# Kernel tuning notes

Hardware: AMD Instinct MI355X
Metric: run time of the kernel (lower is better)

## Reference

```python
import jax, jax.numpy as jnp
import numpy as np
import math

B = 50        # graphs per batch
NPG = 2000    # nodes per graph
EPG = 12000   # edges per graph
F_IN = 256
NHID = 128
RATIO = 0.8


def setup_inputs() -> dict:
    key = jax.random.key(0)
    ks = jax.random.split(key, 12)
    N = B * NPG
    src_loc = jax.random.randint(ks[0], (B, EPG), 0, NPG)
    dst_loc = jax.random.randint(ks[1], (B, EPG), 0, NPG)
    off = (jnp.arange(B) * NPG)[:, None]
    edge_index = jnp.stack([(src_loc + off).reshape(-1), (dst_loc + off).reshape(-1)]).astype(jnp.int32)

    def lin(k, fi, fo):
        return (jax.random.normal(k, (fi, fo), jnp.float32) / np.sqrt(fi).astype(np.float32))

    return {
        "x": jax.random.normal(ks[2], (N, F_IN), jnp.float32),
        "W1": lin(ks[3], F_IN, NHID), "b1": jnp.zeros(NHID, jnp.float32),
        "Ws1": lin(ks[4], NHID, 1), "bs1": jnp.zeros(1, jnp.float32),
        "W2": lin(ks[5], NHID, NHID), "b2": jnp.zeros(NHID, jnp.float32),
        "Ws2": lin(ks[6], NHID, 1), "bs2": jnp.zeros(1, jnp.float32),
        "W3": lin(ks[7], NHID, NHID), "b3": jnp.zeros(NHID, jnp.float32),
        "Ws3": lin(ks[8], NHID, 1), "bs3": jnp.zeros(1, jnp.float32),
        "Wl": lin(ks[9], 2 * NHID, NHID), "bl": jnp.zeros(NHID, jnp.float32),
        "edge_index": edge_index,
    }


def gcn_conv(x, W, b, src, dst, w, N):
    # PyG GCNConv: D^{-1/2} (A + I) D^{-1/2} X W + b, deg from edge weights + self loop
    h = x @ W
    deg = jax.ops.segment_sum(w, dst, num_segments=N) + 1.0
    dis = jax.lax.rsqrt(deg)
    norm = w * dis[src] * dis[dst]                       # [E]
    agg = jax.ops.segment_sum(h[src] * norm[:, None], dst, num_segments=N)
    return agg + h / deg[:, None] + b                    # self-loop norm = 1/deg


def sag_pool(x, src, dst, w, Ws, bs, n_per_graph):
    N = x.shape[0]
    k = math.ceil(RATIO * n_per_graph)
    score = gcn_conv(x, Ws, bs, src, dst, w, N)[:, 0]    # [N]
    _, topi = jax.lax.top_k(score.reshape(B, n_per_graph), k)
    perm = (topi + (jnp.arange(B) * n_per_graph)[:, None]).reshape(-1)
    x_new = x[perm] * jnp.tanh(score[perm])[:, None]
    # filter_adj: keep edges whose endpoints survive, reindex; dropped edges -> weight 0
    mapping = jnp.full((N,), -1, jnp.int32).at[perm].set(jnp.arange(B * k, dtype=jnp.int32))
    ns, nd = mapping[src], mapping[dst]
    valid = (ns >= 0) & (nd >= 0) & (w > 0)
    return (x_new, jnp.where(valid, ns, 0), jnp.where(valid, nd, 0),
            jnp.where(valid, w, jnp.zeros((), x.dtype)), k)


def readout(x, n):
    # global max pool || global mean pool (equal-size graphs, nodes grouped per graph)
    xr = x.reshape(B, n, -1)
    return jnp.concatenate([xr.max(axis=1), xr.mean(axis=1)], axis=-1)


def reference(x, W1, b1, Ws1, bs1, W2, b2, Ws2, bs2, W3, b3, Ws3, bs3, Wl, bl, edge_index):
    src, dst = edge_index[0], edge_index[1]
    w = jnp.ones(src.shape[0], x.dtype)
    n = NPG
    x = jax.nn.relu(gcn_conv(x, W1, b1, src, dst, w, B * n))
    x, src, dst, w, n = sag_pool(x, src, dst, w, Ws1, bs1, n)
    x1 = readout(x, n)
    x = jax.nn.relu(gcn_conv(x, W2, b2, src, dst, w, B * n))
    x, src, dst, w, n = sag_pool(x, src, dst, w, Ws2, bs2, n)
    x2 = readout(x, n)
    x = jax.nn.relu(gcn_conv(x, W3, b3, src, dst, w, B * n))
    x, src, dst, w, n = sag_pool(x, src, dst, w, Ws3, bs3, n)
    x3 = readout(x, n)
    return jax.nn.relu((x1 + x2 + x3) @ Wl + bl)
```

## Files before the change

### kernel.cpp

```cpp
#include <hip/hip_runtime.h>
#include <math.h>

#define B_GRAPHS 50
#define NPG0     2000
#define EPG      12000
#define F_IN_C   256
#define NHID     128
#define N0       (B_GRAPHS * NPG0)
#define NE       (B_GRAPHS * EPG)
#define RSEG     16
#define GSLOTS   7
#define CPAD     136

typedef _Float16 f16x8 __attribute__((ext_vector_type(8)));
typedef float    f32x4 __attribute__((ext_vector_type(4)));

static inline int cdiv(int a, int b) { return (a + b - 1) / b; }

__global__ void k_fill_start(int* __restrict__ cnt, float* __restrict__ accum) {
    int i = blockIdx.x * 256 + threadIdx.x;
    if (i < N0) cnt[i] = 0;
    if (i < B_GRAPHS * 256) accum[i] = 0.f;
}

__global__ void k_init_edges(const int* __restrict__ ei, int* __restrict__ esrc,
                             int* __restrict__ edst, float* __restrict__ ew,
                             int* __restrict__ cnt) {
    int e = blockIdx.x * 256 + threadIdx.x;
    if (e < NE) {
        int d = ei[NE + e];
        esrc[e] = ei[e]; edst[e] = d; ew[e] = 1.0f;
        atomicAdd(&cnt[d], 1);
    }
}

__global__ void k_cvt_all(const float* __restrict__ W1, const float* __restrict__ W2,
                          const float* __restrict__ W3, _Float16* __restrict__ WT1,
                          _Float16* __restrict__ WT2, _Float16* __restrict__ WT3) {
    int t = blockIdx.x * 256 + threadIdx.x;
    if (t < 128 * 256) {
        int n = t >> 8, kk = t & 255;
        WT1[t] = (_Float16)W1[kk * 128 + n];
    } else if (t < 128 * 256 + 128 * 128) {
        int u = t - 32768; int n = u >> 7, kk = u & 127;
        WT2[u] = (_Float16)W2[kk * 128 + n];
    } else {
        int u = t - 49152; int n = u >> 7, kk = u & 127;
        WT3[u] = (_Float16)W3[kk * 128 + n];
    }
}

template<int FP32IN, int F, int GATHER>
__global__ __launch_bounds__(256) void k_gemm_ws(const void* __restrict__ Xin,
                                                 const _Float16* __restrict__ WT,
                                                 const int* __restrict__ perm,
                                                 const float* __restrict__ gate,
                                                 _Float16* __restrict__ H, int N) {
    constexpr int SMEMSZ = (F * 128 > 128 * CPAD) ? F * 128 : 128 * CPAD;
    __shared__ _Float16 smem[SMEMSZ];
    const int tid  = threadIdx.x;
    const int wave = tid >> 6, lane = tid & 63;
    const int quad = lane >> 4, l16 = lane & 15;
    const int m_blk = blockIdx.x * 128;

    constexpr int K8 = F / 8;
#pragma unroll
    for (int c = tid; c < 128 * K8; c += 256) {
        int n = c / K8, k8 = c - n * K8;
        f16x8 v = *(const f16x8*)&WT[(size_t)c * 8];
        *(f16x8*)&smem[n * F + ((k8 ^ (n & 7)) << 3)] = v;
    }
    __syncthreads();

    f32x4 acc[2][8];
#pragma unroll
    for (int i = 0; i < 2; ++i)
#pragma unroll
        for (int j = 0; j < 8; ++j) acc[i][j] = {0.f, 0.f, 0.f, 0.f};

    int row0 = m_blk + wave * 32 + l16;
    int row1 = row0 + 16;
    if (row0 > N - 1) row0 = N - 1;
    if (row1 > N - 1) row1 = N - 1;
    _Float16 g0 = (_Float16)1.0f, g1 = (_Float16)1.0f;
    if (GATHER) {
        g0 = (_Float16)gate[row0]; g1 = (_Float16)gate[row1];
        row0 = perm[row0]; row1 = perm[row1];
    }
    const int sx = l16 & 7;
    constexpr int NKQ = F / 32;

    if (FP32IN) {
        constexpr int PD = (NKQ < 4) ? NKQ : 4;
        const float* base0 = (const float*)Xin + (size_t)row0 * F + quad * 8;
        const float* base1 = (const float*)Xin + (size_t)row1 * F + quad * 8;
        float4 p0[PD][2], p1[PD][2];
#pragma unroll
        for (int i = 0; i < PD; ++i) {
            p0[i][0] = ((const float4*)(base0 + i * 32))[0];
            p0[i][1] = ((const float4*)(base0 + i * 32))[1];
            p1[i][0] = ((const float4*)(base1 + i * 32))[0];
            p1[i][1] = ((const float4*)(base1 + i * 32))[1];
        }
#pragma unroll
        for (int kq = 0; kq < NKQ; ++kq) {
            const int b = kq % PD;
            float4 f0 = p0[b][0], f1 = p0[b][1], h0 = p1[b][0], h1 = p1[b][1];
            if (kq + PD < NKQ) {
                p0[b][0] = ((const float4*)(base0 + (kq + PD) * 32))[0];
                p0[b][1] = ((const float4*)(base0 + (kq + PD) * 32))[1];
                p1[b][0] = ((const float4*)(base1 + (kq + PD) * 32))[0];
                p1[b][1] = ((const float4*)(base1 + (kq + PD) * 32))[1];
            }
            f16x8 af0 = (f16x8){(_Float16)f0.x,(_Float16)f0.y,(_Float16)f0.z,(_Float16)f0.w,
                                (_Float16)f1.x,(_Float16)f1.y,(_Float16)f1.z,(_Float16)f1.w};
            f16x8 af1 = (f16x8){(_Float16)h0.x,(_Float16)h0.y,(_Float16)h0.z,(_Float16)h0.w,
                                (_Float16)h1.x,(_Float16)h1.y,(_Float16)h1.z,(_Float16)h1.w};
            f16x8 bf[8];
#pragma unroll
            for (int j = 0; j < 8; ++j)
                bf[j] = *(const f16x8*)&smem[(j * 16 + l16) * F + ((((kq << 2) + quad) ^ sx) << 3)];
#pragma unroll
            for (int j = 0; j < 8; ++j) {
                acc[0][j] = __builtin_amdgcn_mfma_f32_16x16x32_f16(af0, bf[j], acc[0][j], 0, 0, 0);
                acc[1][j] = __builtin_amdgcn_mfma_f32_16x16x32_f16(af1, bf[j], acc[1][j], 0, 0, 0);
            }
        }
    } else {
        const _Float16* base0 = (const _Float16*)Xin + (size_t)row0 * F + quad * 8;
        const _Float16* base1 = (const _Float16*)Xin + (size_t)row1 * F + quad * 8;
        f16x8 q0[NKQ], q1[NKQ];
#pragma unroll
        for (int i = 0; i < NKQ; ++i) {
            q0[i] = *(const f16x8*)(base0 + i * 32);
            q1[i] = *(const f16x8*)(base1 + i * 32);
        }
#pragma unroll
        for (int kq = 0; kq < NKQ; ++kq) {
            f16x8 af0 = q0[kq], af1 = q1[kq];
            if (GATHER) { af0 = af0 * g0; af1 = af1 * g1; }
            f16x8 bf[8];
#pragma unroll
            for (int j = 0; j < 8; ++j)
                bf[j] = *(const f16x8*)&smem[(j * 16 + l16) * F + ((((kq << 2) + quad) ^ sx) << 3)];
#pragma unroll
            for (int j = 0; j < 8; ++j) {
                acc[0][j] = __builtin_amdgcn_mfma_f32_16x16x32_f16(af0, bf[j], acc[0][j], 0, 0, 0);
                acc[1][j] = __builtin_amdgcn_mfma_f32_16x16x32_f16(af1, bf[j], acc[1][j], 0, 0, 0);
            }
        }
    }
    __syncthreads();

    _Float16* sC = smem;
    const int rw = wave * 32;
#pragma unroll
    for (int i = 0; i < 2; ++i)
#pragma unroll
        for (int j = 0; j < 8; ++j)
#pragma unroll
            for (int g = 0; g < 4; ++g)
                sC[(rw + i * 16 + quad * 4 + g) * CPAD + j * 16 + l16] = (_Float16)acc[i][j][g];
    __syncthreads();
    {
        int rr = tid >> 1;
        int gr = m_blk + rr;
        if (gr < N) {
            _Float16* Hr = H + (size_t)gr * 128 + (tid & 1) * 64;
            const _Float16* Sr = sC + rr * CPAD + (tid & 1) * 64;
#pragma unroll
            for (int c = 0; c < 8; ++c)
                *(f16x8*)&Hr[c * 8] = *(const f16x8*)&Sr[c * 8];
        }
    }
}

__global__ __launch_bounds__(256) void k_scan(const int* __restrict__ cnt,
                                              int* __restrict__ offs,
                                              int* __restrict__ cursor, int npg) {
    __shared__ int ch[256];
    int b = blockIdx.x, tid = threadIdx.x;
    int per = (npg + 255) >> 8;
    int base = b * npg;
    int s0 = tid * per;
    int s1 = s0 + per; if (s1 > npg) s1 = npg; if (s0 > npg) s0 = npg;
    int s = 0;
    for (int i = s0; i < s1; ++i) s += cnt[base + i];
    ch[tid] = s;
    __syncthreads();
    for (int d = 1; d < 256; d <<= 1) {
        int t = ch[tid] + ((tid >= d) ? ch[tid - d] : 0);
        __syncthreads();
        ch[tid] = t;
        __syncthreads();
    }
    int run = b * EPG + ch[tid] - s;
    for (int i = s0; i < s1; ++i) {
        offs[base + i] = run; cursor[base + i] = run;
        run += cnt[base + i];
    }
}

__global__ void k_fill_csr(const int* __restrict__ esrc, const int* __restrict__ edst,
                           const float* __restrict__ ew, const int* __restrict__ cnt,
                           int* __restrict__ cursor, int* __restrict__ csr_src,
                           float* __restrict__ csr_norm) {
    int e = blockIdx.x * 256 + threadIdx.x;
    if (e < NE) {
        if (ew[e] > 0.f) {
            int sN = esrc[e], d = edst[e];
            int pos = atomicAdd(&cursor[d], 1);
            csr_src[pos] = sN;
            csr_norm[pos] = rsqrtf((float)(cnt[sN] + 1)) * rsqrtf((float)(cnt[d] + 1));
        }
    }
}

__global__ __launch_bounds__(256) void k_agg(const _Float16* __restrict__ H,
                                             const int* __restrict__ csr_src,
                                             const float* __restrict__ csr_norm,
                                             const int* __restrict__ offs,
                                             const int* __restrict__ cnt,
                                             const float* __restrict__ bias,
                                             const float* __restrict__ Ws,
                                             _Float16* __restrict__ X,
                                             float* __restrict__ hs,
                                             int bpg, int npg) {
    int bi = blockIdx.x;
    int x = bi & 7, s = bi >> 3;
    int gslot = s / bpg, blk = s - gslot * bpg;
    int g = x + 8 * gslot;
    if (g >= B_GRAPHS) return;
    int node = g * npg + blk * 4 + (threadIdx.x >> 6);
    int lane = threadIdx.x & 63;
    int quad = lane >> 4, l16 = lane & 15;

    int st = offs[node], c = cnt[node], en = st + c;
    float acc[8];
#pragma unroll
    for (int j = 0; j < 8; ++j) acc[j] = 0.f;

    if (c > 0) {
        for (int e0 = st; e0 < en; e0 += 8) {
            int eA = e0 + quad, eB = eA + 4;
            int ecA = eA < en ? eA : en - 1;
            int ecB = eB < en ? eB : en - 1;
            int uA = csr_src[ecA], uB = csr_src[ecB];
            float nA = (eA < en) ? csr_norm[ecA] : 0.f;
            float nB = (eB < en) ? csr_norm[ecB] : 0.f;
            f16x8 hA = *(const f16x8*)&H[(size_t)uA * NHID + l16 * 8];
            f16x8 hB = *(const f16x8*)&H[(size_t)uB * NHID + l16 * 8];
#pragma unroll
            for (int j = 0; j < 8; ++j) acc[j] = fmaf((float)hA[j], nA, acc[j]);
#pragma unroll
            for (int j = 0; j < 8; ++j) acc[j] = fmaf((float)hB[j], nB, acc[j]);
        }
    }
#pragma unroll
    for (int j = 0; j < 8; ++j) {
        acc[j] += __shfl_xor(acc[j], 16, 64);
        acc[j] += __shfl_xor(acc[j], 32, 64);
    }
    float invd = 1.f / (float)(c + 1);
    f16x8 hn = *(const f16x8*)&H[(size_t)node * NHID + l16 * 8];
    float4 b0 = *(const float4*)&bias[l16 * 8];
    float4 b1 = *(const float4*)&bias[l16 * 8 + 4];
    float4 w0 = *(const float4*)&Ws[l16 * 8];
    float4 w1 = *(const float4*)&Ws[l16 * 8 + 4];
    const float bb[8] = {b0.x, b0.y, b0.z, b0.w, b1.x, b1.y, b1.z, b1.w};
    const float ww[8] = {w0.x, w0.y, w0.z, w0.w, w1.x, w1.y, w1.z, w1.w};
    float sd = 0.f;
    f16x8 o;
#pragma unroll
    for (int j = 0; j < 8; ++j) {
        float v = fmaxf(acc[j] + (float)hn[j] * invd + bb[j], 0.f);
        o[j] = (_Float16)v;
        sd = fmaf(v, ww[j], sd);
    }
    if (quad == 0)
        *(f16x8*)&X[(size_t)node * NHID + l16 * 8] = o;
    sd += __shfl_xor(sd, 1, 64);
    sd += __shfl_xor(sd, 2, 64);
    sd += __shfl_xor(sd, 4, 64);
    sd += __shfl_xor(sd, 8, 64);
    if (lane == 0) hs[node] = sd;
}

__global__ void k_score(const float* __restrict__ hs, const int* __restrict__ csr_src,
                        const float* __restrict__ csr_norm, const int* __restrict__ offs,
                        const int* __restrict__ cnt, const float* __restrict__ bs,
                        float* __restrict__ score, int N) {
    int i = blockIdx.x * 256 + threadIdx.x;
    if (i >= N) return;
    int s = offs[i], c = cnt[i];
    float a = 0.f;
    for (int e = s; e < s + c; ++e) a = fmaf(hs[csr_src[e]], csr_norm[e], a);
    score[i] = a + hs[i] / (float)(c + 1) + bs[0];
}

__global__ __launch_bounds__(1024) void k_topk(const float* __restrict__ score,
                                               int* __restrict__ mapping,
                                               int* __restrict__ perm,
                                               float* __restrict__ gate,
                                               int* __restrict__ cntN,
                                               int npg, int k) {
    __shared__ float ss[2048];
    __shared__ int   si[2048];
    int b = blockIdx.x, tid = threadIdx.x;
    for (int i = tid; i < 2048; i += 1024) {
        if (i < npg) { ss[i] = score[b * npg + i]; si[i] = i; }
        else         { ss[i] = -__builtin_inff();  si[i] = i; }
    }
    __syncthreads();
    for (int size = 2; size <= 2048; size <<= 1) {
        for (int stride = size >> 1; stride > 0; stride >>= 1) {
            int t = tid;
            int i = ((t & ~(stride - 1)) << 1) | (t & (stride - 1));
            int j = i | stride;
            float sa = ss[i], sb = ss[j];
            int   ia = si[i], ib = si[j];
            bool b_before_a = (sb > sa) || (sb == sa && ib < ia);
            bool forward = ((i & size) == 0);
            bool doswap = forward ? b_before_a : !b_before_a;
            if (doswap) { ss[i] = sb; ss[j] = sa; si[i] = ib; si[j] = ia; }
            __syncthreads();
        }
    }
    for (int j = tid; j < npg; j += 1024) {
        int oldg = b * npg + si[j];
        if (j < k) {
            int newg = b * k + j;
            perm[newg] = oldg;
            mapping[oldg] = newg;
            gate[newg] = tanhf(ss[j]);
        } else {
            mapping[oldg] = -1;
        }
    }
    for (int j = tid; j < k; j += 1024) cntN[b * k + j] = 0;
}

__global__ __launch_bounds__(128) void k_pool_readout(const _Float16* __restrict__ X,
                                                      const float* __restrict__ gate,
                                                      const int* __restrict__ perm,
                                                      float* __restrict__ pmax,
                                                      float* __restrict__ psum, int k) {
    int s = blockIdx.x, b = blockIdx.y, f = threadIdx.x;
    int j0 = (k * s) / RSEG, j1 = (k * (s + 1)) / RSEG;
    float mx = -__builtin_inff(), sm = 0.f;
    for (int j = j0; j < j1; ++j) {
        int g = b * k + j;
        int old = perm[g];
        float v = (float)X[(size_t)old * NHID + f] * gate[g];
        mx = fmaxf(mx, v);
        sm += v;
    }
    pmax[(size_t)(b * RSEG + s) * NHID + f] = mx;
    psum[(size_t)(b * RSEG + s) * NHID + f] = sm;
}

__global__ __launch_bounds__(128) void k_readout_comb(const float* __restrict__ pmax,
                                                      const float* __restrict__ psum,
                                                      float* __restrict__ accum, int k) {
    int b = blockIdx.x, f = threadIdx.x;
    float mx = -__builtin_inff(), sm = 0.f;
#pragma unroll
    for (int s = 0; s < RSEG; ++s) {
        mx = fmaxf(mx, pmax[(size_t)(b * RSEG + s) * NHID + f]);
        sm += psum[(size_t)(b * RSEG + s) * NHID + f];
    }
    accum[b * 256 + f]       += mx;
    accum[b * 256 + 128 + f] += sm / (float)k;
}

__global__ void k_remap(int* __restrict__ esrc, int* __restrict__ edst,
                        float* __restrict__ ew, const int* __restrict__ mapping,
                        int* __restrict__ cntN) {
    int e = blockIdx.x * 256 + threadIdx.x;
    if (e >= NE) return;
    int sN = esrc[e], d = edst[e];
    float we = ew[e];
    int ns = mapping[sN], nd = mapping[d];
    bool valid = (ns >= 0) && (nd >= 0) && (we > 0.f);
    esrc[e] = valid ? ns : 0;
    edst[e] = valid ? nd : 0;
    ew[e] = valid ? we : 0.f;
    if (valid) atomicAdd(&cntN[nd], 1);
}

__global__ __launch_bounds__(128) void k_comb_final(const float* __restrict__ pmax,
                                                    const float* __restrict__ psum,
                                                    const float* __restrict__ accum,
                                                    const float* __restrict__ Wl,
                                                    const float* __restrict__ bl,
                                                    float* __restrict__ out, int k) {
    __shared__ float a[256];
    int b = blockIdx.x, f = threadIdx.x;
    float mx = -__builtin_inff(), sm = 0.f;
#pragma unroll
    for (int s = 0; s < RSEG; ++s) {
        mx = fmaxf(mx, pmax[(size_t)(b * RSEG + s) * NHID + f]);
        sm += psum[(size_t)(b * RSEG + s) * NHID + f];
    }
    a[f]       = accum[b * 256 + f] + mx;
    a[128 + f] = accum[b * 256 + 128 + f] + sm / (float)k;
    __syncthreads();
    float s = bl[f];
    for (int i = 0; i < 256; ++i) s = fmaf(a[i], Wl[i * NHID + f], s);
    out[b * NHID + f] = fmaxf(s, 0.f);
}

extern "C" void kernel_launch(void* const* d_in, const int* in_sizes, int n_in,
                              void* d_out, int out_size, void* d_ws, size_t ws_size,
                              hipStream_t stream) {
    const float* x0 = (const float*)d_in[0];
    const float* Wm[3] = {(const float*)d_in[1], (const float*)d_in[5], (const float*)d_in[9]};
    const float* bm[3] = {(const float*)d_in[2], (const float*)d_in[6], (const float*)d_in[10]};
    const float* Wsc[3] = {(const float*)d_in[3], (const float*)d_in[7], (const float*)d_in[11]};
    const float* bsc[3] = {(const float*)d_in[4], (const float*)d_in[8], (const float*)d_in[12]};
    const float* Wl = (const float*)d_in[13];
    const float* bl = (const float*)d_in[14];
    const int*   ei = (const int*)d_in[15];
    float* out = (float*)d_out;

    _Float16* bufA = (_Float16*)d_ws;
    _Float16* bufB = bufA + (size_t)N0 * NHID;
    _Float16* WT1  = bufB + (size_t)N0 * NHID;
    _Float16* WT2  = WT1 + 128 * 256;
    _Float16* WT3  = WT2 + 128 * 128;
    float* hs     = (float*)(WT3 + 128 * 128);
    float* score  = hs + N0;
    float* gate   = score + N0;
    float* accum  = gate + N0;
    float* pmax   = accum + B_GRAPHS * 256;
    float* psum   = pmax + B_GRAPHS * RSEG * NHID;
    int*   cntA   = (int*)(psum + B_GRAPHS * RSEG * NHID);
    int*   cntB   = cntA + N0;
    int*   offs   = cntB + N0;
    int*   cursor = offs + N0;
    int*   mapping= cursor + N0;
    int*   perm   = mapping + N0;
    int*   esrc   = perm + N0;
    int*   edst   = esrc + NE;
    float* ew     = (float*)(edst + NE);
    int*   csr_src= (int*)(ew + NE);
    float* csr_norm = (float*)(csr_src + NE);

    _Float16* WTs[3] = {WT1, WT2, WT3};
    const int EG = cdiv(NE, 256);

    k_fill_start<<<cdiv(N0, 256), 256, 0, stream>>>(cntA, accum);
    k_init_edges<<<EG, 256, 0, stream>>>(ei, esrc, edst, ew, cntA);
    k_cvt_all<<<256, 256, 0, stream>>>(Wm[0], Wm[1], Wm[2], WT1, WT2, WT3);

    int npg = NPG0;
    _Float16* Hbuf = bufA; _Float16* Xbuf = bufB;

    for (int layer = 0; layer < 3; ++layer) {
        int N = B_GRAPHS * npg;
        int k = (npg * 4) / 5;
        int NG = cdiv(N, 256);
        int bpg = npg >> 2;
        int* cnt  = (layer == 1) ? cntB : cntA;
        int* cntN = (layer == 1) ? cntA : cntB;

        if (layer == 0)
            k_gemm_ws<1, 256, 0><<<cdiv(N, 128), 256, 0, stream>>>(x0, WTs[0], perm, gate, Hbuf, N);
        else
            k_gemm_ws<0, 128, 1><<<cdiv(N, 128), 256, 0, stream>>>(Xbuf, WTs[layer], perm, gate, Hbuf, N);
        k_scan<<<B_GRAPHS, 256, 0, stream>>>(cnt, offs, cursor, npg);
        k_fill_csr<<<EG, 256, 0, stream>>>(esrc, edst, ew, cnt, cursor, csr_src, csr_norm);
        k_agg<<<8 * GSLOTS * bpg, 256, 0, stream>>>(Hbuf, csr_src, csr_norm, offs, cnt,
                                                    bm[layer], Wsc[layer], Xbuf, hs, bpg, npg);
        k_score<<<NG, 256, 0, stream>>>(hs, csr_src, csr_norm, offs, cnt, bsc[layer], score, N);
        k_topk<<<B_GRAPHS, 1024, 0, stream>>>(score, mapping, perm, gate, cntN, npg, k);
        k_pool_readout<<<dim3(RSEG, B_GRAPHS), 128, 0, stream>>>(Xbuf, gate, perm, pmax, psum, k);
        if (layer < 2) {
            k_remap<<<EG, 256, 0, stream>>>(esrc, edst, ew, mapping, cntN);
            k_readout_comb<<<B_GRAPHS, 128, 0, stream>>>(pmax, psum, accum, k);
        } else {
            k_comb_final<<<B_GRAPHS, 128, 0, stream>>>(pmax, psum, accum, Wl, bl, out, k);
        }

        npg = k;
    }
}
```

Measured before the change: 647.8 us.

## Split weight staging into K halves to shrink LDS and raise occupancy

For the F=256 layer, the transposed weight tile is now staged into shared memory in two 128-wide K halves, with a barrier-protected reload halfway through the K loop, instead of all at once. This halves the shared-memory footprint to the size of the output staging buffer, and the launch bounds now request 4 blocks per SM. Weight loads are also issued after the activation prefetch so they can overlap with it. The cost is extra barriers and a second weight load per block, and the register cap may cause spills.

```diff
diff --git a/kernel.cpp b/kernel.cpp
--- a/kernel.cpp
+++ b/kernel.cpp
@@ -51,26 +51,19 @@
 }
 
 template<int FP32IN, int F, int GATHER>
-__global__ __launch_bounds__(256) void k_gemm_ws(const void* __restrict__ Xin,
-                                                 const _Float16* __restrict__ WT,
-                                                 const int* __restrict__ perm,
-                                                 const float* __restrict__ gate,
-                                                 _Float16* __restrict__ H, int N) {
-    constexpr int SMEMSZ = (F * 128 > 128 * CPAD) ? F * 128 : 128 * CPAD;
+__global__ __launch_bounds__(256, 4) void k_gemm_ws(const void* __restrict__ Xin,
+                                                    const _Float16* __restrict__ WT,
+                                                    const int* __restrict__ perm,
+                                                    const float* __restrict__ gate,
+                                                    _Float16* __restrict__ H, int N) {
+    constexpr int KH  = (F > 128) ? 128 : F;
+    constexpr int K8H = KH / 8;
+    constexpr int SMEMSZ = (128 * KH > 128 * CPAD) ? 128 * KH : 128 * CPAD;
     __shared__ _Float16 smem[SMEMSZ];
     const int tid  = threadIdx.x;
     const int wave = tid >> 6, lane = tid & 63;
     const int quad = lane >> 4, l16 = lane & 15;
     const int m_blk = blockIdx.x * 128;
-
-    constexpr int K8 = F / 8;
-#pragma unroll
-    for (int c = tid; c < 128 * K8; c += 256) {
-        int n = c / K8, k8 = c - n * K8;
-        f16x8 v = *(const f16x8*)&WT[(size_t)c * 8];
-        *(f16x8*)&smem[n * F + ((k8 ^ (n & 7)) << 3)] = v;
-    }
-    __syncthreads();
 
     f32x4 acc[2][8];
 #pragma unroll
@@ -103,7 +96,24 @@
             p1[i][1] = ((const float4*)(base1 + i * 32))[1];
         }
 #pragma unroll
+        for (int c = tid; c < 128 * K8H; c += 256) {
+            int n = c / K8H, k8 = c - n * K8H;
+            f16x8 v = *(const f16x8*)&WT[(size_t)(n * (F / 8) + k8) * 8];
+            *(f16x8*)&smem[n * KH + ((k8 ^ (n & 7)) << 3)] = v;
+        }
+        __syncthreads();
+#pragma unroll
         for (int kq = 0; kq < NKQ; ++kq) {
+            if (KH < F && kq == NKQ / 2) {
+                __syncthreads();
+#pragma unroll
+                for (int c = tid; c < 128 * K8H; c += 256) {
+                    int n = c / K8H, k8 = c - n * K8H;
+                    f16x8 v = *(const f16x8*)&WT[(size_t)(n * (F / 8) + K8H + k8) * 8];
+                    *(f16x8*)&smem[n * KH + ((k8 ^ (n & 7)) << 3)] = v;
+                }
+                __syncthreads();
+            }
             const int b = kq % PD;
             float4 f0 = p0[b][0], f1 = p0[b][1], h0 = p1[b][0], h1 = p1[b][1];
             if (kq + PD < NKQ) {
@@ -119,7 +129,7 @@
             f16x8 bf[8];
 #pragma unroll
             for (int j = 0; j < 8; ++j)
-                bf[j] = *(const f16x8*)&smem[(j * 16 + l16) * F + ((((kq << 2) + quad) ^ sx) << 3)];
+                bf[j] = *(const f16x8*)&smem[(j * 16 + l16) * KH + (((((kq & 3) << 2) + quad) ^ sx) << 3)];
 #pragma unroll
             for (int j = 0; j < 8; ++j) {
                 acc[0][j] = __builtin_amdgcn_mfma_f32_16x16x32_f16(af0, bf[j], acc[0][j], 0, 0, 0);
@@ -127,6 +137,12 @@
             }
         }
     } else {
+#pragma unroll
+        for (int c = tid; c < 128 * K8H; c += 256) {
+            int n = c / K8H, k8 = c - n * K8H;
+            f16x8 v = *(const f16x8*)&WT[(size_t)(n * K8H + k8) * 8];
+            *(f16x8*)&smem[n * KH + ((k8 ^ (n & 7)) << 3)] = v;
+        }
         const _Float16* base0 = (const _Float16*)Xin + (size_t)row0 * F + quad * 8;
         const _Float16* base1 = (const _Float16*)Xin + (size_t)row1 * F + quad * 8;
         f16x8 q0[NKQ], q1[NKQ];
@@ -135,6 +151,7 @@
             q0[i] = *(const f16x8*)(base0 + i * 32);
             q1[i] = *(const f16x8*)(base1 + i * 32);
         }
+        __syncthreads();
 #pragma unroll
         for (int kq = 0; kq < NKQ; ++kq) {
             f16x8 af0 = q0[kq], af1 = q1[kq];
@@ -142,7 +159,7 @@
             f16x8 bf[8];
 #pragma unroll
             for (int j = 0; j < 8; ++j)
-                bf[j] = *(const f16x8*)&smem[(j * 16 + l16) * F + ((((kq << 2) + quad) ^ sx) << 3)];
+                bf[j] = *(const f16x8*)&smem[(j * 16 + l16) * KH + (((((kq & 3) << 2) + quad) ^ sx) << 3)];
 #pragma unroll
             for (int j = 0; j < 8; ++j) {
                 acc[0][j] = __builtin_amdgcn_mfma_f32_16x16x32_f16(af0, bf[j], acc[0][j], 0, 0, 0);
```

Result: no change. 654.4 us (+1.0%).
